# Optimization experiments

Hardware: AMD Instinct MI355X
Metric: run time of the kernel (lower is better)

The kernel has to match this reference:

```python
import jax, jax.numpy as jnp
import numpy as np

D = 1024
H = 16
HD = D // H


def setup_inputs() -> dict:
    key = jax.random.key(0)
    k1, k2, k3 = jax.random.split(key, 3)
    x = jax.random.normal(k1, (4, 2048, D), dtype=jnp.float32)
    # torch Linear weight is [out, in]; we store transposed [in, out] for x @ W
    w_qkv = jax.random.normal(k2, (D, 3 * D), dtype=jnp.float32) * (1.0 / np.sqrt(D))
    w_o = jax.random.normal(k3, (D, D), dtype=jnp.float32) * (1.0 / np.sqrt(D))
    return {"x": x, "w_qkv": w_qkv, "w_o": w_o}


def reference(x, w_qkv, w_o):
    B, T, _ = x.shape
    qkv = x @ w_qkv                                  # [B, T, 3D]
    q, k, v = jnp.split(qkv, 3, axis=-1)
    def heads(t):
        return t.reshape(B, T, H, HD).transpose(0, 2, 1, 3)  # [B, H, T, hd]
    q, k, v = heads(q), heads(k), heads(v)
    scale = 1.0 / jnp.sqrt(jnp.asarray(HD, x.dtype))
    att = jnp.einsum("bhtd,bhsd->bhts", q, k) * scale       # [B, H, T, T]
    att = jax.nn.softmax(att, axis=-1)
    y = jnp.einsum("bhts,bhsd->bhtd", att, v)                # [B, H, T, hd]
    y = y.transpose(0, 2, 1, 3).reshape(B, T, D)
    return y @ w_o
```

## Files before the change

### kernel.cpp

```cpp
#include <hip/hip_runtime.h>
#include <hip/hip_bf16.h>
#include <stdint.h>

typedef __attribute__((ext_vector_type(8))) short short8;
typedef __attribute__((ext_vector_type(4))) float f32x4;

#define MFMA_BF16(a, b, c) __builtin_amdgcn_mfma_f32_16x16x32_bf16((a), (b), (c), 0, 0, 0)

#define QSCALE 0.18033688011118293f

__device__ __forceinline__ unsigned short f2bf(float f) {
  unsigned int u = __builtin_bit_cast(unsigned int, f);
  u += 0x7fffu + ((u >> 16) & 1u);
  return (unsigned short)(u >> 16);
}

__device__ __forceinline__ uint32_t pkbf(float a, float b) {
  float2 f; f.x = a; f.y = b;
  __hip_bfloat162 h = __float22bfloat162_rn(f);
  uint32_t u;
  __builtin_memcpy(&u, &h, 4);
  return u;
}

__device__ __forceinline__ float exp2_fast(float x) {
#if __has_builtin(__builtin_amdgcn_exp2f)
  return __builtin_amdgcn_exp2f(x);
#else
  float r;
  asm("v_exp_f32 %0, %1" : "=v"(r) : "v"(x));
  return r;
#endif
}

__device__ __forceinline__ void gload_lds16(const void* g, void* l) {
  __builtin_amdgcn_global_load_lds(
      (const __attribute__((address_space(1))) unsigned int*)g,
      (__attribute__((address_space(3))) unsigned int*)l, 16, 0, 0);
}

__global__ __launch_bounds__(256) void cvt_f32_bf16_k(const float* __restrict__ in,
                                                      unsigned short* __restrict__ out,
                                                      int n8) {
  int i = blockIdx.x * 256 + threadIdx.x;
  if (i >= n8) return;
  const float4* p = (const float4*)(in + (size_t)i * 8);
  float4 a = p[0], b = p[1];
  short8 o;
  o[0] = (short)f2bf(a.x); o[1] = (short)f2bf(a.y);
  o[2] = (short)f2bf(a.z); o[3] = (short)f2bf(a.w);
  o[4] = (short)f2bf(b.x); o[5] = (short)f2bf(b.y);
  o[6] = (short)f2bf(b.z); o[7] = (short)f2bf(b.w);
  *(short8*)(out + (size_t)i * 8) = o;
}

__global__ __launch_bounds__(256) void transpose_f32_bf16_k(const float* __restrict__ in,
                                                            unsigned short* __restrict__ out,
                                                            int R, int C) {
  __shared__ __attribute__((aligned(16))) unsigned short t[64][65];
  int c0 = blockIdx.x * 64, r0 = blockIdx.y * 64;
  int tx = threadIdx.x;
  for (int rr = threadIdx.y; rr < 64; rr += 4)
    t[rr][tx] = f2bf(in[(size_t)(r0 + rr) * C + c0 + tx]);
  __syncthreads();
  for (int rr = threadIdx.y; rr < 64; rr += 4)
    out[(size_t)(c0 + rr) * R + r0 + tx] = t[tx][rr];
}

template <int MODE>
__global__ __launch_bounds__(256, 3) void gemm_bt_k(
    const unsigned short* __restrict__ A, const unsigned short* __restrict__ Bt,
    float* __restrict__ Cout, unsigned short* __restrict__ Qd,
    unsigned short* __restrict__ Kd, unsigned short* __restrict__ Vtd,
    int M, int N, int Kdim) {
  __shared__ __attribute__((aligned(16))) unsigned short As[3][4096];
  __shared__ __attribute__((aligned(16))) unsigned short Bs[3][4096];
  const int tid = threadIdx.x, lane = tid & 63, w = tid >> 6;
  const int wr = w >> 1, wc = w & 1;
  const int lo = lane & 15, hi = lane >> 4;
  const int tm = blockIdx.y, tn = blockIdx.x;
  f32x4 acc[4][4] = {};
  const char* Ab = (const char*)A;
  const char* Bb = (const char*)Bt;
  const int nk = Kdim >> 5;

#define GSTAGE(kt, bb)                                                        \
  {                                                                           \
    _Pragma("unroll") for (int j = 0; j < 2; ++j) {                           \
      int o8 = w * 2048 + j * 1024 + lane * 16;                               \
      int src = o8 ^ (((o8 >> 6) & 3) << 4);                                  \
      int row = src >> 6, cb = src & 63;                                      \
      gload_lds16(Ab + ((size_t)(tm * 128 + row) * Kdim + (kt) * 32) * 2 + cb,\
                  (char*)As[bb] + o8);                                        \
      gload_lds16(Bb + ((size_t)(tn * 128 + row) * Kdim + (kt) * 32) * 2 + cb,\
                  (char*)Bs[bb] + o8);                                        \
    }                                                                         \
  }

  GSTAGE(0, 0);
  GSTAGE(1, 1);
  asm volatile("s_waitcnt vmcnt(4)" ::: "memory");
  __builtin_amdgcn_s_barrier();
  int gbuf = 0;
  for (int kt = 0; kt < nk; ++kt) {
    if (kt + 2 < nk) {
      int nb = gbuf + 2; if (nb >= 3) nb -= 3;
      GSTAGE(kt + 2, nb);
    }
    short8 af[4], bf[4];
#pragma unroll
    for (int m = 0; m < 4; ++m) {
      int r = wr * 64 + m * 16 + lo;
      int ad = (r * 64 + hi * 16) ^ ((r & 3) << 4);
      af[m] = *(const short8*)((const char*)As[gbuf] + ad);
    }
#pragma unroll
    for (int n = 0; n < 4; ++n) {
      int r = wc * 64 + n * 16 + lo;
      int ad = (r * 64 + hi * 16) ^ ((r & 3) << 4);
      bf[n] = *(const short8*)((const char*)Bs[gbuf] + ad);
    }
    __builtin_amdgcn_s_setprio(1);
#pragma unroll
    for (int m = 0; m < 4; ++m)
#pragma unroll
      for (int n = 0; n < 4; ++n)
        acc[m][n] = MFMA_BF16(af[m], bf[n], acc[m][n]);
    __builtin_amdgcn_s_setprio(0);
    if (kt + 2 < nk)
      asm volatile("s_waitcnt vmcnt(4)" ::: "memory");
    else
      asm volatile("s_waitcnt vmcnt(0)" ::: "memory");
    __builtin_amdgcn_s_barrier();
    gbuf = (gbuf + 1 == 3) ? 0 : gbuf + 1;
  }
  if (MODE == 1) {
#pragma unroll
    for (int m = 0; m < 4; ++m)
#pragma unroll
      for (int n = 0; n < 4; ++n)
#pragma unroll
        for (int j = 0; j < 4; ++j) {
          int row = tm * 128 + wr * 64 + m * 16 + hi * 4 + j;
          int col = tn * 128 + wc * 64 + n * 16 + lo;
          Cout[(size_t)row * N + col] = acc[m][n][j];
        }
  } else {
    int which = (tn * 128) >> 10;
#pragma unroll
    for (int m = 0; m < 4; ++m)
#pragma unroll
      for (int n = 0; n < 4; ++n)
#pragma unroll
        for (int j = 0; j < 4; ++j) {
          int row = tm * 128 + wr * 64 + m * 16 + hi * 4 + j;
          int col = tn * 128 + wc * 64 + n * 16 + lo;
          int b = row >> 11, t = row & 2047;
          int rem = col & 1023;
          int h = rem >> 6, hd = rem & 63;
          float v = acc[m][n][j];
          if (which == 0)
            Qd[((size_t)(b * 16 + h) * 2048 + t) * 64 + hd] = f2bf(v * QSCALE);
          else if (which == 1)
            Kd[((size_t)(b * 16 + h) * 2048 + t) * 64 + hd] = f2bf(v);
          else
            Vtd[((size_t)(b * 16 + h) * 64 + hd) * 2048 + t] = f2bf(v);
        }
  }
}

__global__ __launch_bounds__(512) void attn_k(const unsigned short* __restrict__ Qd,
                                              const unsigned short* __restrict__ Kd,
                                              const unsigned short* __restrict__ Vtd,
                                              unsigned short* __restrict__ Y) {
  const int T = 2048, NT = 32;
  int flat = blockIdx.x;
  int qt = (flat >> 3) & 7;
  int bh = (flat & 7) * 8 + (flat >> 6);
  int tid = threadIdx.x, lane = tid & 63, w = tid >> 6;
  int lo = lane & 15, hi = lane >> 4;
  const unsigned short* Qbh = Qd + (size_t)bh * T * 64;
  const char* Kb = (const char*)(Kd + (size_t)bh * T * 64);
  const char* Vb = (const char*)(Vtd + (size_t)bh * 64 * T);

  __shared__ __attribute__((aligned(16))) unsigned short Ks[3][4096];
  __shared__ __attribute__((aligned(16))) unsigned short Vs[3][4096];
  __shared__ __attribute__((aligned(16))) unsigned short Ps[8][2][1024];

  const short8 ones = {0x3F80, 0x3F80, 0x3F80, 0x3F80,
                       0x3F80, 0x3F80, 0x3F80, 0x3F80};

  short8 qf[2][2];
#pragma unroll
  for (int qh = 0; qh < 2; ++qh) {
    const unsigned short* qrow =
        Qbh + (size_t)(qt * 256 + w * 32 + qh * 16 + lo) * 64 + hi * 8;
    qf[qh][0] = *(const short8*)qrow;
    qf[qh][1] = *(const short8*)(qrow + 32);
  }
  f32x4 oacc[2][4] = {};
  f32x4 lacc[2] = {};

#define STAGE(kt, b)                                                          \
  {                                                                           \
    int base = w * 1024;                                                      \
    int o8 = base + lane * 16;                                                \
    int src = o8 ^ (((o8 >> 7) & 7) << 4);                                    \
    gload_lds16(Kb + (size_t)(kt) * 8192 + src, (char*)Ks[b] + base);         \
    int hd_ = src >> 7, cbyt = src & 127;                                     \
    gload_lds16(Vb + (size_t)hd_ * (T * 2) + (size_t)(kt) * 128 + cbyt,       \
                (char*)Vs[b] + base);                                         \
  }

  STAGE(0, 0);
  STAGE(1, 1);
  asm volatile("s_waitcnt vmcnt(2)" ::: "memory");
  __builtin_amdgcn_s_barrier();
  int bufc = 0;
  for (int kt = 0; kt < NT; ++kt) {
    if (kt + 2 < NT) {
      int nb = bufc + 2; if (nb >= 3) nb -= 3;
      STAGE(kt + 2, nb);
    }

    f32x4 sacc[2][4] = {};
    __builtin_amdgcn_s_setprio(1);
#pragma unroll
    for (int st = 0; st < 4; ++st)
#pragma unroll
      for (int c = 0; c < 2; ++c) {
        int row = st * 16 + lo;
        int addr = (row * 128 + c * 64 + hi * 16) ^ ((row & 7) << 4);
        short8 kf = *(const short8*)((const char*)Ks[bufc] + addr);
        sacc[0][st] = MFMA_BF16(kf, qf[0][c], sacc[0][st]);
        sacc[1][st] = MFMA_BF16(kf, qf[1][c], sacc[1][st]);
      }
    __builtin_amdgcn_s_setprio(0);

#pragma unroll
    for (int qh = 0; qh < 2; ++qh) {
      char* pw = (char*)&Ps[w][qh][0];
#pragma unroll
      for (int st = 0; st < 4; ++st) {
        float p0 = exp2_fast(sacc[qh][st][0]);
        float p1 = exp2_fast(sacc[qh][st][1]);
        float p2 = exp2_fast(sacc[qh][st][2]);
        float p3 = exp2_fast(sacc[qh][st][3]);
        int wb = (lo * 128 + st * 32 + hi * 8) ^ ((lo & 7) << 4);
        *(uint32_t*)(pw + wb) = pkbf(p0, p1);
        *(uint32_t*)(pw + wb + 4) = pkbf(p2, p3);
      }
    }

    __builtin_amdgcn_s_setprio(1);
#pragma unroll
    for (int c = 0; c < 2; ++c) {
      int pb = (lo * 128 + c * 64 + hi * 16) ^ ((lo & 7) << 4);
      short8 pf0 = *(const short8*)((const char*)&Ps[w][0][0] + pb);
      short8 pf1 = *(const short8*)((const char*)&Ps[w][1][0] + pb);
      lacc[0] = MFMA_BF16(pf0, ones, lacc[0]);
      lacc[1] = MFMA_BF16(pf1, ones, lacc[1]);
#pragma unroll
      for (int n = 0; n < 4; ++n) {
        int row = n * 16 + lo;
        int addr = (row * 128 + c * 64 + hi * 16) ^ ((row & 7) << 4);
        short8 vf = *(const short8*)((const char*)Vs[bufc] + addr);
        oacc[0][n] = MFMA_BF16(pf0, vf, oacc[0][n]);
        oacc[1][n] = MFMA_BF16(pf1, vf, oacc[1][n]);
      }
    }
    __builtin_amdgcn_s_setprio(0);

    if (kt + 2 < NT)
      asm volatile("s_waitcnt vmcnt(2)" ::: "memory");
    else
      asm volatile("s_waitcnt vmcnt(0)" ::: "memory");
    __builtin_amdgcn_s_barrier();
    bufc = (bufc + 1 == 3) ? 0 : bufc + 1;
  }

  int b = bh >> 4, h = bh & 15;
#pragma unroll
  for (int qh = 0; qh < 2; ++qh)
#pragma unroll
    for (int r = 0; r < 4; ++r) {
      int t = qt * 256 + w * 32 + qh * 16 + hi * 4 + r;
      float rl = 1.0f / lacc[qh][r];
#pragma unroll
      for (int n = 0; n < 4; ++n) {
        int hd = n * 16 + lo;
        Y[((size_t)(b * 2048 + t)) * 1024 + h * 64 + hd] =
            f2bf(oacc[qh][n][r] * rl);
      }
    }
}

extern "C" void kernel_launch(void* const* d_in, const int* in_sizes, int n_in,
                              void* d_out, int out_size, void* d_ws, size_t ws_size,
                              hipStream_t stream) {
  const float* x = (const float*)d_in[0];
  const float* w_qkv = (const float*)d_in[1];
  const float* w_o = (const float*)d_in[2];
  float* out = (float*)d_out;
  char* ws = (char*)d_ws;
  unsigned short* xb    = (unsigned short*)(ws + 0);
  unsigned short* wqkvT = (unsigned short*)(ws + 16777216);
  unsigned short* woT   = (unsigned short*)(ws + 23068672);
  unsigned short* qb    = (unsigned short*)(ws + 25165824);
  unsigned short* kb    = (unsigned short*)(ws + 41943040);
  unsigned short* vtb   = (unsigned short*)(ws + 58720256);
  unsigned short* yb    = xb;

  cvt_f32_bf16_k<<<4096, 256, 0, stream>>>(x, xb, 1048576);
  transpose_f32_bf16_k<<<dim3(48, 16), dim3(64, 4), 0, stream>>>(w_qkv, wqkvT, 1024, 3072);
  transpose_f32_bf16_k<<<dim3(16, 16), dim3(64, 4), 0, stream>>>(w_o, woT, 1024, 1024);
  gemm_bt_k<0><<<dim3(24, 64), 256, 0, stream>>>(xb, wqkvT, nullptr, qb, kb, vtb,
                                                 8192, 3072, 1024);
  attn_k<<<512, 512, 0, stream>>>(qb, kb, vtb, yb);
  gemm_bt_k<1><<<dim3(8, 64), 256, 0, stream>>>(yb, woT, out, nullptr, nullptr, nullptr,
                                                8192, 1024, 1024);
}
```

Measured before the change: 215.6 us.

## Enlarge GEMM tiles to 256x128 with 8 waves and K=64 interleaved prefetch

The bf16 GEMM kernel moves from a 128x128 tile with 4 waves and K-step 32 to a 256x128 tile with 8 waves and K-step 64. Each K-step is split into four sub-phases, and the global-to-LDS prefetch for two stages ahead is spread across those phases, with a swizzle widened to 8 rows. The goal is more operand reuse per LDS byte and fewer loop iterations and barriers per unit of work. In exchange, LDS use rises to 144KB per block, which drops occupancy to one block per CU, and barriers are added inside each K-step. The grid halves, so the out-projection GEMM launches only 256 blocks.

```diff
diff --git a/kernel.cpp b/kernel.cpp
--- a/kernel.cpp
+++ b/kernel.cpp
@@ -68,13 +68,13 @@
 }
 
 template <int MODE>
-__global__ __launch_bounds__(256, 3) void gemm_bt_k(
+__global__ __launch_bounds__(512) void gemm_bt_k(
     const unsigned short* __restrict__ A, const unsigned short* __restrict__ Bt,
     float* __restrict__ Cout, unsigned short* __restrict__ Qd,
     unsigned short* __restrict__ Kd, unsigned short* __restrict__ Vtd,
     int M, int N, int Kdim) {
-  __shared__ __attribute__((aligned(16))) unsigned short As[3][4096];
-  __shared__ __attribute__((aligned(16))) unsigned short Bs[3][4096];
+  __shared__ __attribute__((aligned(16))) unsigned short As[3][16384];
+  __shared__ __attribute__((aligned(16))) unsigned short Bs[3][8192];
   const int tid = threadIdx.x, lane = tid & 63, w = tid >> 6;
   const int wr = w >> 1, wc = w & 1;
   const int lo = lane & 15, hi = lane >> 4;
@@ -82,66 +82,84 @@
   f32x4 acc[4][4] = {};
   const char* Ab = (const char*)A;
   const char* Bb = (const char*)Bt;
-  const int nk = Kdim >> 5;
-
-#define GSTAGE(kt, bb)                                                        \
+  const int nkt = Kdim >> 6;
+
+#define GS1(kt, bb, s)                                                        \
   {                                                                           \
-    _Pragma("unroll") for (int j = 0; j < 2; ++j) {                           \
-      int o8 = w * 2048 + j * 1024 + lane * 16;                               \
-      int src = o8 ^ (((o8 >> 6) & 3) << 4);                                  \
-      int row = src >> 6, cb = src & 63;                                      \
-      gload_lds16(Ab + ((size_t)(tm * 128 + row) * Kdim + (kt) * 32) * 2 + cb,\
+    if ((s) < 4) {                                                            \
+      int o8 = (s) * 8192 + tid * 16;                                         \
+      int src = o8 ^ (((o8 >> 7) & 7) << 4);                                  \
+      int row = src >> 7, cb = src & 127;                                     \
+      gload_lds16(Ab + ((size_t)(tm * 256 + row) * Kdim + (kt) * 64) * 2 + cb,\
                   (char*)As[bb] + o8);                                        \
-      gload_lds16(Bb + ((size_t)(tn * 128 + row) * Kdim + (kt) * 32) * 2 + cb,\
+    } else {                                                                  \
+      int o8 = ((s) - 4) * 8192 + tid * 16;                                   \
+      int src = o8 ^ (((o8 >> 7) & 7) << 4);                                  \
+      int row = src >> 7, cb = src & 127;                                     \
+      gload_lds16(Bb + ((size_t)(tn * 128 + row) * Kdim + (kt) * 64) * 2 + cb,\
                   (char*)Bs[bb] + o8);                                        \
     }                                                                         \
   }
-
-  GSTAGE(0, 0);
-  GSTAGE(1, 1);
-  asm volatile("s_waitcnt vmcnt(4)" ::: "memory");
+#define GS6(kt, bb) { GS1(kt, bb, 0) GS1(kt, bb, 1) GS1(kt, bb, 2)            \
+                      GS1(kt, bb, 3) GS1(kt, bb, 4) GS1(kt, bb, 5) }
+
+  GS6(0, 0);
+  GS6(1, 1);
+  asm volatile("s_waitcnt vmcnt(6)" ::: "memory");
   __builtin_amdgcn_s_barrier();
   int gbuf = 0;
-  for (int kt = 0; kt < nk; ++kt) {
-    if (kt + 2 < nk) {
-      int nb = gbuf + 2; if (nb >= 3) nb -= 3;
-      GSTAGE(kt + 2, nb);
-    }
-    short8 af[4], bf[4];
-#pragma unroll
-    for (int m = 0; m < 4; ++m) {
-      int r = wr * 64 + m * 16 + lo;
-      int ad = (r * 64 + hi * 16) ^ ((r & 3) << 4);
-      af[m] = *(const short8*)((const char*)As[gbuf] + ad);
-    }
-#pragma unroll
-    for (int n = 0; n < 4; ++n) {
-      int r = wc * 64 + n * 16 + lo;
-      int ad = (r * 64 + hi * 16) ^ ((r & 3) << 4);
-      bf[n] = *(const short8*)((const char*)Bs[gbuf] + ad);
-    }
-    __builtin_amdgcn_s_setprio(1);
+  for (int kt = 0; kt < nkt; ++kt) {
+    int nb = gbuf + 2; if (nb >= 3) nb -= 3;
+    const bool pf = (kt + 2 < nkt);
+    const char* Ap = (const char*)As[gbuf];
+    const char* Bp = (const char*)Bs[gbuf];
+#pragma unroll
+    for (int p = 0; p < 4; ++p) {
+      if (pf && p < 3) { GS1(kt + 2, nb, 2 * p) GS1(kt + 2, nb, 2 * p + 1) }
+      int mq = p & 1, nq = p >> 1;
+      short8 af[2][2], bf[2][2];
+#pragma unroll
+      for (int i = 0; i < 2; ++i)
+#pragma unroll
+        for (int c = 0; c < 2; ++c) {
+          int ra = wr * 64 + (mq * 2 + i) * 16 + lo;
+          af[i][c] = *(const short8*)(Ap + ((ra * 128 + c * 64 + hi * 16) ^
+                                            ((ra & 7) << 4)));
+          int rb = wc * 64 + (nq * 2 + i) * 16 + lo;
+          bf[i][c] = *(const short8*)(Bp + ((rb * 128 + c * 64 + hi * 16) ^
+                                            ((rb & 7) << 4)));
+        }
+      __builtin_amdgcn_s_setprio(1);
+#pragma unroll
+      for (int i = 0; i < 2; ++i)
+#pragma unroll
+        for (int j = 0; j < 2; ++j) {
+          acc[mq * 2 + i][nq * 2 + j] =
+              MFMA_BF16(af[i][0], bf[j][0], acc[mq * 2 + i][nq * 2 + j]);
+          acc[mq * 2 + i][nq * 2 + j] =
+              MFMA_BF16(af[i][1], bf[j][1], acc[mq * 2 + i][nq * 2 + j]);
+        }
+      __builtin_amdgcn_s_setprio(0);
+      if (p < 3) {
+        __builtin_amdgcn_s_barrier();
+      } else {
+        if (pf)
+          asm volatile("s_waitcnt vmcnt(6)" ::: "memory");
+        else
+          asm volatile("s_waitcnt vmcnt(0)" ::: "memory");
+        __builtin_amdgcn_s_barrier();
+      }
+    }
+    gbuf = (gbuf + 1 == 3) ? 0 : gbuf + 1;
+  }
+  if (MODE == 1) {
 #pragma unroll
     for (int m = 0; m < 4; ++m)
 #pragma unroll
       for (int n = 0; n < 4; ++n)
-        acc[m][n] = MFMA_BF16(af[m], bf[n], acc[m][n]);
-    __builtin_amdgcn_s_setprio(0);
-    if (kt + 2 < nk)
-      asm volatile("s_waitcnt vmcnt(4)" ::: "memory");
-    else
-      asm volatile("s_waitcnt vmcnt(0)" ::: "memory");
-    __builtin_amdgcn_s_barrier();
-    gbuf = (gbuf + 1 == 3) ? 0 : gbuf + 1;
-  }
-  if (MODE == 1) {
-#pragma unroll
-    for (int m = 0; m < 4; ++m)
-#pragma unroll
-      for (int n = 0; n < 4; ++n)
 #pragma unroll
         for (int j = 0; j < 4; ++j) {
-          int row = tm * 128 + wr * 64 + m * 16 + hi * 4 + j;
+          int row = tm * 256 + wr * 64 + m * 16 + hi * 4 + j;
           int col = tn * 128 + wc * 64 + n * 16 + lo;
           Cout[(size_t)row * N + col] = acc[m][n][j];
         }
@@ -153,7 +171,7 @@
       for (int n = 0; n < 4; ++n)
 #pragma unroll
         for (int j = 0; j < 4; ++j) {
-          int row = tm * 128 + wr * 64 + m * 16 + hi * 4 + j;
+          int row = tm * 256 + wr * 64 + m * 16 + hi * 4 + j;
           int col = tn * 128 + wc * 64 + n * 16 + lo;
           int b = row >> 11, t = row & 2047;
           int rem = col & 1023;
@@ -314,9 +332,9 @@
   cvt_f32_bf16_k<<<4096, 256, 0, stream>>>(x, xb, 1048576);
   transpose_f32_bf16_k<<<dim3(48, 16), dim3(64, 4), 0, stream>>>(w_qkv, wqkvT, 1024, 3072);
   transpose_f32_bf16_k<<<dim3(16, 16), dim3(64, 4), 0, stream>>>(w_o, woT, 1024, 1024);
-  gemm_bt_k<0><<<dim3(24, 64), 256, 0, stream>>>(xb, wqkvT, nullptr, qb, kb, vtb,
+  gemm_bt_k<0><<<dim3(24, 32), 512, 0, stream>>>(xb, wqkvT, nullptr, qb, kb, vtb,
                                                  8192, 3072, 1024);
   attn_k<<<512, 512, 0, stream>>>(qb, kb, vtb, yb);
-  gemm_bt_k<1><<<dim3(8, 64), 256, 0, stream>>>(yb, woT, out, nullptr, nullptr, nullptr,
+  gemm_bt_k<1><<<dim3(8, 32), 512, 0, stream>>>(yb, woT, out, nullptr, nullptr, nullptr,
                                                 8192, 1024, 1024);
 }
```

After: 271.2 us. 1.26x slower.
